# Optimization experiments

Measured on AMD Instinct MI355X. Metric: run time of the kernel, lower is better.

## Reference

```python
import jax, jax.numpy as jnp
import numpy as np

DIM = 1024
EXPERT_DIM = 2048
N_EXPERTS = 2
B, T = 4, 2048


def setup_inputs() -> dict:
    key = jax.random.key(0)
    ks = jax.random.split(key, 10)
    s = 0.02
    return {
        "x": jax.random.normal(ks[0], (B, T, DIM), dtype=jnp.float32),
        "W_router": jax.random.normal(ks[1], (DIM, N_EXPERTS), dtype=jnp.float32) * s,
        "router_bias": jnp.zeros((N_EXPERTS,), dtype=jnp.float32),
        "Wg": jax.random.normal(ks[2], (N_EXPERTS, DIM, EXPERT_DIM), dtype=jnp.float32) * s,
        "Wu": jax.random.normal(ks[3], (N_EXPERTS, DIM, EXPERT_DIM), dtype=jnp.float32) * s,
        "Wd": jax.random.normal(ks[4], (N_EXPERTS, EXPERT_DIM, DIM), dtype=jnp.float32) * s,
        "Sg": jax.random.normal(ks[5], (DIM, EXPERT_DIM), dtype=jnp.float32) * s,
        "Su": jax.random.normal(ks[6], (DIM, EXPERT_DIM), dtype=jnp.float32) * s,
        "Sd": jax.random.normal(ks[7], (EXPERT_DIM, DIM), dtype=jnp.float32) * s,
    }


def reference(x, W_router, router_bias, Wg, Wu, Wd, Sg, Su, Sd):
    Bc, Tc, D = x.shape
    flat = x.reshape(Bc * Tc, D)                               # [N, D]
    logits = flat @ W_router                                   # [N, E]
    scores = jax.nn.softmax(logits, axis=-1)
    hard = jax.nn.one_hot(jnp.argmax(logits + router_bias, axis=-1),
                          W_router.shape[1], dtype=flat.dtype)  # [N, E]
    # straight-through weights: forward value == hard, grad flows via scores
    ste = hard + scores - jax.lax.stop_gradient(scores)
    w = jnp.where(hard > 0.5, ste, jnp.zeros_like(ste))         # mask w > 0.5 (== argmax expert)
    # routed SwiGLU experts (top-1 hard routing; unselected rows weighted 0)
    g = jax.nn.silu(jnp.einsum('nd,edf->enf', flat, Wg))        # [E, N, F]
    u = jnp.einsum('nd,edf->enf', flat, Wu)
    y = jnp.einsum('enf,efd->end', g * u, Wd)                   # [E, N, D]
    routed = jnp.einsum('ne,end->nd', w, y)                     # [N, D]
    # always-active shared SwiGLU expert
    shared = (jax.nn.silu(flat @ Sg) * (flat @ Su)) @ Sd        # [N, D]
    return (routed + shared).reshape(Bc, Tc, D)
```

## Files before the change

### kernel.cpp

```cpp
#include <hip/hip_runtime.h>
#include <stdint.h>

#define NTOK 8192
#define DIM 1024
#define EDIM 2048

typedef __attribute__((ext_vector_type(8))) short bf16x8;
typedef __attribute__((ext_vector_type(4))) float f32x4;

__device__ __forceinline__ unsigned short f2bf(float f) {
  union { float f; unsigned u; } v; v.f = f;
  unsigned r = (v.u + 0x7FFF + ((v.u >> 16) & 1)) >> 16;
  return (unsigned short)r;
}

__device__ __forceinline__ void gload16(const void* g, void* l) {
  __builtin_amdgcn_global_load_lds(
      (const __attribute__((address_space(1))) unsigned int*)g,
      (__attribute__((address_space(3))) unsigned int*)l, 16, 0, 0);
}

__global__ void cvtrouter_k(const float* __restrict__ x, const float* __restrict__ Wr,
                            const float* __restrict__ bias,
                            unsigned short* __restrict__ xb, int* __restrict__ choice) {
  const int wid = threadIdx.x >> 6, lane = threadIdx.x & 63;
  const float b0 = bias[0], b1 = bias[1];
  const float2* wr = (const float2*)Wr;
  #pragma unroll
  for (int r = 0; r < 2; ++r) {
    const int n = blockIdx.x * 8 + wid * 2 + r;
    const float4* xr = (const float4*)(x + (size_t)n * DIM);
    uint2* xo = (uint2*)(xb + (size_t)n * DIM);
    float s0 = 0.f, s1 = 0.f;
    #pragma unroll
    for (int i = 0; i < 4; ++i) {
      const int idx = i * 64 + lane;
      float4 v = xr[idx];
      float2 wa = wr[idx * 4], wb = wr[idx * 4 + 1], wc = wr[idx * 4 + 2], wd = wr[idx * 4 + 3];
      s0 += v.x * wa.x + v.y * wb.x + v.z * wc.x + v.w * wd.x;
      s1 += v.x * wa.y + v.y * wb.y + v.z * wc.y + v.w * wd.y;
      union { unsigned short s[4]; uint2 u; } o;
      o.s[0] = f2bf(v.x); o.s[1] = f2bf(v.y); o.s[2] = f2bf(v.z); o.s[3] = f2bf(v.w);
      xo[idx] = o.u;
    }
    #pragma unroll
    for (int off = 32; off; off >>= 1) {
      s0 += __shfl_xor(s0, off);
      s1 += __shfl_xor(s1, off);
    }
    if (lane == 0) choice[n] = (s1 + b1 > s0 + b0) ? 1 : 0;
  }
}

__global__ void scan_k(const int* __restrict__ choice, int* __restrict__ counts,
                       int* __restrict__ rowlist) {
  const int t = threadIdx.x;
  const int base = t * 8;
  int c[8]; int ones = 0;
  #pragma unroll
  for (int j = 0; j < 8; ++j) { c[j] = choice[base + j]; ones += c[j]; }
  const int lane = t & 63, wid = t >> 6;
  int v = ones;
  #pragma unroll
  for (int off = 1; off < 64; off <<= 1) {
    int o = __shfl_up(v, off);
    if (lane >= off) v += o;
  }
  __shared__ int wsum[16];
  if (lane == 63) wsum[wid] = v;
  __syncthreads();
  int pre = 0, tot = 0;
  #pragma unroll
  for (int w = 0; w < 16; ++w) {
    int s = wsum[w];
    if (w < wid) pre += s;
    tot += s;
  }
  const int excl = pre + v - ones;
  int p0 = base - excl;
  int p1 = excl;
  #pragma unroll
  for (int j = 0; j < 8; ++j) {
    if (c[j]) rowlist[NTOK + p1++] = base + j;
    else rowlist[p0++] = base + j;
  }
  if (t == 0) { counts[0] = NTOK - tot; counts[1] = tot; }
}

__global__ void trans_k(const float* __restrict__ Sg, const float* __restrict__ Su,
                        const float* __restrict__ Sd, const float* __restrict__ Wg,
                        const float* __restrict__ Wu, const float* __restrict__ Wd,
                        unsigned short* __restrict__ wt) {
  const int id = blockIdx.y;
  const size_t MSZ = (size_t)DIM * EDIM;
  const float* src; int R, C;
  switch (id) {
    case 0: src = Sg;       R = DIM;  C = EDIM; break;
    case 1: src = Su;       R = DIM;  C = EDIM; break;
    case 2: src = Sd;       R = EDIM; C = DIM;  break;
    case 3: src = Wg;       R = DIM;  C = EDIM; break;
    case 4: src = Wg + MSZ; R = DIM;  C = EDIM; break;
    case 5: src = Wu;       R = DIM;  C = EDIM; break;
    case 6: src = Wu + MSZ; R = DIM;  C = EDIM; break;
    case 7: src = Wd;       R = EDIM; C = DIM;  break;
    default: src = Wd + MSZ; R = EDIM; C = DIM;  break;
  }
  unsigned short* dst = wt + (size_t)id * MSZ;
  __shared__ float tile[32][33];
  int tC = C >> 5;
  int tr = blockIdx.x / tC, tc = blockIdx.x % tC;
  int xt = threadIdx.x, yt = threadIdx.y;
  #pragma unroll
  for (int j = 0; j < 4; ++j)
    tile[yt + j * 8][xt] = src[(size_t)(tr * 32 + yt + j * 8) * C + tc * 32 + xt];
  __syncthreads();
  #pragma unroll
  for (int j = 0; j < 4; ++j)
    dst[(size_t)(tc * 32 + yt + j * 8) * R + tr * 32 + xt] = f2bf(tile[xt][yt + j * 8]);
}

template<bool GATHER>
__global__ __launch_bounds__(256, 2)
void up_k(const unsigned short* __restrict__ xb, const unsigned short* __restrict__ Bg0,
          const unsigned short* __restrict__ Bu0, const int* __restrict__ counts,
          const int* __restrict__ rowlist, unsigned short* __restrict__ h) {
  int mt, cnt;
  const int* rl = nullptr;
  const unsigned short* Bg = Bg0;
  const unsigned short* Bu = Bu0;
  if (GATHER) {
    int e = blockIdx.x >> 6;
    mt = blockIdx.x & 63;
    cnt = counts[e];
    if (mt * 128 >= cnt) return;
    rl = rowlist + e * NTOK;
    size_t off = (size_t)e * ((size_t)DIM * EDIM);
    Bg = Bg0 + off; Bu = Bu0 + off;
  } else { mt = blockIdx.x; cnt = NTOK; }

  const int t = threadIdx.x;
  const int lane = t & 63;
  const int wm = t >> 7, wn = (t >> 6) & 1;
  const int m0 = mt * 128, n0 = blockIdx.y * 128;

  __shared__ __align__(16) unsigned char lA[16384];
  __shared__ __align__(16) unsigned char lBg[16384];
  __shared__ __align__(16) unsigned char lBu[16384];

  size_t aoff[4], boff[4];
  int dsto[4];
  #pragma unroll
  for (int i = 0; i < 4; ++i) {
    int flat = i * 4096 + t * 16;
    int row = flat >> 7;
    int kb = (flat & 127) ^ ((row & 7) << 4);
    int ar = m0 + row;
    if (GATHER) ar = rl[ar < cnt ? ar : cnt - 1];
    aoff[i] = (size_t)ar * (DIM * 2) + kb;
    boff[i] = (size_t)(n0 + row) * (DIM * 2) + kb;
    dsto[i] = flat;
  }

  f32x4 accg[4][4], accu[4][4];
  #pragma unroll
  for (int i = 0; i < 4; ++i)
    #pragma unroll
    for (int j = 0; j < 4; ++j) {
      accg[i][j] = f32x4{0.f, 0.f, 0.f, 0.f};
      accu[i][j] = f32x4{0.f, 0.f, 0.f, 0.f};
    }

  const char* xc = (const char*)xb;
  const char* gc = (const char*)Bg;
  const char* uc = (const char*)Bu;

  for (int kt = 0; kt < DIM / 64; ++kt) {
    __syncthreads();
    size_t ko = (size_t)kt * 128;
    #pragma unroll
    for (int i = 0; i < 4; ++i) {
      gload16(xc + aoff[i] + ko, lA + dsto[i]);
      gload16(gc + boff[i] + ko, lBg + dsto[i]);
      gload16(uc + boff[i] + ko, lBu + dsto[i]);
    }
    __syncthreads();
    #pragma unroll
    for (int ks = 0; ks < 2; ++ks) {
      bf16x8 af[4], bgf[4], buf_[4];
      int kb = ks * 64 + ((lane >> 4) << 4);
      #pragma unroll
      for (int mi = 0; mi < 4; ++mi) {
        int row = wm * 64 + mi * 16 + (lane & 15);
        af[mi] = *(const bf16x8*)(lA + row * 128 + (kb ^ ((row & 7) << 4)));
      }
      #pragma unroll
      for (int ni = 0; ni < 4; ++ni) {
        int col = wn * 64 + ni * 16 + (lane & 15);
        int o = col * 128 + (kb ^ ((col & 7) << 4));
        bgf[ni] = *(const bf16x8*)(lBg + o);
        buf_[ni] = *(const bf16x8*)(lBu + o);
      }
      #pragma unroll
      for (int mi = 0; mi < 4; ++mi)
        #pragma unroll
        for (int ni = 0; ni < 4; ++ni) {
          accg[mi][ni] = __builtin_amdgcn_mfma_f32_16x16x32_bf16(af[mi], bgf[ni], accg[mi][ni], 0, 0, 0);
          accu[mi][ni] = __builtin_amdgcn_mfma_f32_16x16x32_bf16(af[mi], buf_[ni], accu[mi][ni], 0, 0, 0);
        }
    }
  }

  #pragma unroll
  for (int mi = 0; mi < 4; ++mi) {
    #pragma unroll
    for (int r = 0; r < 4; ++r) {
      int pr = m0 + wm * 64 + mi * 16 + ((lane >> 4) << 2) + r;
      if (GATHER && pr >= cnt) continue;
      int tok = GATHER ? rl[pr] : pr;
      unsigned short* hrow = h + (size_t)tok * EDIM;
      #pragma unroll
      for (int ni = 0; ni < 4; ++ni) {
        int col = n0 + wn * 64 + ni * 16 + (lane & 15);
        float g = accg[mi][ni][r], u = accu[mi][ni][r];
        float s = g / (1.f + __expf(-g));
        hrow[col] = f2bf(s * u);
      }
    }
  }
}

template<bool GATHER>
__global__ __launch_bounds__(256, 2)
void down_k(const unsigned short* __restrict__ hb, const unsigned short* __restrict__ Bd0,
            const int* __restrict__ counts, const int* __restrict__ rowlist,
            float* __restrict__ out) {
  int mt, cnt;
  const int* rl = nullptr;
  const unsigned short* Bd = Bd0;
  if (GATHER) {
    int e = blockIdx.x >> 6;
    mt = blockIdx.x & 63;
    cnt = counts[e];
    if (mt * 128 >= cnt) return;
    rl = rowlist + e * NTOK;
    Bd = Bd0 + (size_t)e * ((size_t)DIM * EDIM);
  } else { mt = blockIdx.x; cnt = NTOK; }

  const int t = threadIdx.x;
  const int lane = t & 63;
  const int wm = t >> 7, wn = (t >> 6) & 1;
  const int m0 = mt * 128, n0 = blockIdx.y * 128;

  __shared__ __align__(16) unsigned char lA[16384];
  __shared__ __align__(16) unsigned char lB[16384];

  size_t aoff[4], boff[4];
  int dsto[4];
  #pragma unroll
  for (int i = 0; i < 4; ++i) {
    int flat = i * 4096 + t * 16;
    int row = flat >> 7;
    int kb = (flat & 127) ^ ((row & 7) << 4);
    int ar = m0 + row;
    if (GATHER) ar = rl[ar < cnt ? ar : cnt - 1];
    aoff[i] = (size_t)ar * (EDIM * 2) + kb;
    boff[i] = (size_t)(n0 + row) * (EDIM * 2) + kb;
    dsto[i] = flat;
  }

  f32x4 acc[4][4];
  #pragma unroll
  for (int i = 0; i < 4; ++i)
    #pragma unroll
    for (int j = 0; j < 4; ++j) acc[i][j] = f32x4{0.f, 0.f, 0.f, 0.f};

  const char* ac = (const char*)hb;
  const char* bc = (const char*)Bd;

  for (int kt = 0; kt < EDIM / 64; ++kt) {
    __syncthreads();
    size_t ko = (size_t)kt * 128;
    #pragma unroll
    for (int i = 0; i < 4; ++i) {
      gload16(ac + aoff[i] + ko, lA + dsto[i]);
      gload16(bc + boff[i] + ko, lB + dsto[i]);
    }
    __syncthreads();
    #pragma unroll
    for (int ks = 0; ks < 2; ++ks) {
      bf16x8 af[4], bf[4];
      int kb = ks * 64 + ((lane >> 4) << 4);
      #pragma unroll
      for (int mi = 0; mi < 4; ++mi) {
        int row = wm * 64 + mi * 16 + (lane & 15);
        af[mi] = *(const bf16x8*)(lA + row * 128 + (kb ^ ((row & 7) << 4)));
      }
      #pragma unroll
      for (int ni = 0; ni < 4; ++ni) {
        int col = wn * 64 + ni * 16 + (lane & 15);
        bf[ni] = *(const bf16x8*)(lB + col * 128 + (kb ^ ((col & 7) << 4)));
      }
      #pragma unroll
      for (int mi = 0; mi < 4; ++mi)
        #pragma unroll
        for (int ni = 0; ni < 4; ++ni)
          acc[mi][ni] = __builtin_amdgcn_mfma_f32_16x16x32_bf16(af[mi], bf[ni], acc[mi][ni], 0, 0, 0);
    }
  }

  #pragma unroll
  for (int mi = 0; mi < 4; ++mi) {
    #pragma unroll
    for (int r = 0; r < 4; ++r) {
      int pr = m0 + wm * 64 + mi * 16 + ((lane >> 4) << 2) + r;
      if (GATHER && pr >= cnt) continue;
      int tok = GATHER ? rl[pr] : pr;
      float* orow = out + (size_t)tok * DIM;
      #pragma unroll
      for (int ni = 0; ni < 4; ++ni) {
        int col = n0 + wn * 64 + ni * 16 + (lane & 15);
        float v = acc[mi][ni][r];
        if (GATHER) orow[col] += v; else orow[col] = v;
      }
    }
  }
}

extern "C" void kernel_launch(void* const* d_in, const int* in_sizes, int n_in,
                              void* d_out, int out_size, void* d_ws, size_t ws_size,
                              hipStream_t stream) {
  const float* x  = (const float*)d_in[0];
  const float* Wr = (const float*)d_in[1];
  const float* rb = (const float*)d_in[2];
  const float* Wg = (const float*)d_in[3];
  const float* Wu = (const float*)d_in[4];
  const float* Wd = (const float*)d_in[5];
  const float* Sg = (const float*)d_in[6];
  const float* Su = (const float*)d_in[7];
  const float* Sd = (const float*)d_in[8];
  float* out = (float*)d_out;

  const size_t MSZ = (size_t)DIM * EDIM;
  char* ws = (char*)d_ws;
  int* counts  = (int*)ws;
  int* choice  = (int*)(ws + 256);
  int* rowlist = (int*)(ws + 256 + 32768);
  unsigned short* xb = (unsigned short*)(ws + 256 + 32768 + 65536);
  unsigned short* wt = xb + (size_t)NTOK * DIM;
  unsigned short* h  = wt + 9 * MSZ;

  const unsigned short* Sgt = wt + 0 * MSZ;
  const unsigned short* Sut = wt + 1 * MSZ;
  const unsigned short* Sdt = wt + 2 * MSZ;
  const unsigned short* Wgt = wt + 3 * MSZ;
  const unsigned short* Wut = wt + 5 * MSZ;
  const unsigned short* Wdt = wt + 7 * MSZ;

  cvtrouter_k<<<1024, 256, 0, stream>>>(x, Wr, rb, xb, choice);
  scan_k<<<1, 1024, 0, stream>>>(choice, counts, rowlist);
  trans_k<<<dim3(2048, 9), dim3(32, 8), 0, stream>>>(Sg, Su, Sd, Wg, Wu, Wd, wt);

  up_k<false><<<dim3(64, 16), 256, 0, stream>>>(xb, Sgt, Sut, nullptr, nullptr, h);
  down_k<false><<<dim3(64, 8), 256, 0, stream>>>(h, Sdt, nullptr, nullptr, out);
  up_k<true><<<dim3(128, 16), 256, 0, stream>>>(xb, Wgt, Wut, counts, rowlist, h);
  down_k<true><<<dim3(128, 8), 256, 0, stream>>>(h, Wdt, counts, rowlist, out);
}
```

Measured before the change: 284.3 us.

## Replace GEMM kernels with double-buffered 256-row tiled kernel and interleaved gate/up weights

```diff
diff --git a/kernel.cpp b/kernel.cpp
--- a/kernel.cpp
+++ b/kernel.cpp
@@ -19,6 +19,9 @@
       (const __attribute__((address_space(1))) unsigned int*)g,
       (__attribute__((address_space(3))) unsigned int*)l, 16, 0, 0);
 }
+
+#define BARRIER() do { __builtin_amdgcn_s_barrier(); asm volatile("" ::: "memory"); } while (0)
+#define VMW(n) asm volatile("s_waitcnt vmcnt(" #n ")" ::: "memory")
 
 __global__ void cvtrouter_k(const float* __restrict__ x, const float* __restrict__ Wr,
                             const float* __restrict__ bias,
@@ -93,19 +96,19 @@
                         unsigned short* __restrict__ wt) {
   const int id = blockIdx.y;
   const size_t MSZ = (size_t)DIM * EDIM;
-  const float* src; int R, C;
+  const float* src; int R, C, type; size_t dof;
   switch (id) {
-    case 0: src = Sg;       R = DIM;  C = EDIM; break;
-    case 1: src = Su;       R = DIM;  C = EDIM; break;
-    case 2: src = Sd;       R = EDIM; C = DIM;  break;
-    case 3: src = Wg;       R = DIM;  C = EDIM; break;
-    case 4: src = Wg + MSZ; R = DIM;  C = EDIM; break;
-    case 5: src = Wu;       R = DIM;  C = EDIM; break;
-    case 6: src = Wu + MSZ; R = DIM;  C = EDIM; break;
-    case 7: src = Wd;       R = EDIM; C = DIM;  break;
-    default: src = Wd + MSZ; R = EDIM; C = DIM;  break;
-  }
-  unsigned short* dst = wt + (size_t)id * MSZ;
+    case 0: src = Sg;       R = DIM;  C = EDIM; type = 0; dof = 0;        break;
+    case 1: src = Su;       R = DIM;  C = EDIM; type = 1; dof = 0;        break;
+    case 2: src = Wg;       R = DIM;  C = EDIM; type = 0; dof = 2 * MSZ;  break;
+    case 3: src = Wu;       R = DIM;  C = EDIM; type = 1; dof = 2 * MSZ;  break;
+    case 4: src = Wg + MSZ; R = DIM;  C = EDIM; type = 0; dof = 4 * MSZ;  break;
+    case 5: src = Wu + MSZ; R = DIM;  C = EDIM; type = 1; dof = 4 * MSZ;  break;
+    case 6: src = Sd;       R = EDIM; C = DIM;  type = 2; dof = 6 * MSZ;  break;
+    case 7: src = Wd;       R = EDIM; C = DIM;  type = 2; dof = 7 * MSZ;  break;
+    default: src = Wd + MSZ; R = EDIM; C = DIM; type = 2; dof = 8 * MSZ;  break;
+  }
+  unsigned short* dst = wt + dof;
   __shared__ float tile[32][33];
   int tC = C >> 5;
   int tr = blockIdx.x / tC, tc = blockIdx.x % tC;
@@ -115,212 +118,207 @@
     tile[yt + j * 8][xt] = src[(size_t)(tr * 32 + yt + j * 8) * C + tc * 32 + xt];
   __syncthreads();
   #pragma unroll
-  for (int j = 0; j < 4; ++j)
-    dst[(size_t)(tc * 32 + yt + j * 8) * R + tr * 32 + xt] = f2bf(tile[xt][yt + j * 8]);
-}
-
-template<bool GATHER>
-__global__ __launch_bounds__(256, 2)
-void up_k(const unsigned short* __restrict__ xb, const unsigned short* __restrict__ Bg0,
-          const unsigned short* __restrict__ Bu0, const int* __restrict__ counts,
-          const int* __restrict__ rowlist, unsigned short* __restrict__ h) {
-  int mt, cnt;
+  for (int j = 0; j < 4; ++j) {
+    int f = tc * 32 + yt + j * 8;
+    int row = (type == 2) ? f : (((f >> 4) << 5) + (f & 15) + (type ? 16 : 0));
+    dst[(size_t)row * R + tr * 32 + xt] = f2bf(tile[xt][yt + j * 8]);
+  }
+}
+
+template<int BN, int KDIM, bool GATHER, int EPI>
+__global__ __launch_bounds__(512, 2)
+void gemm_k(const unsigned short* __restrict__ A, const unsigned short* __restrict__ B0,
+            const int* __restrict__ counts, const int* __restrict__ rowlist,
+            unsigned short* __restrict__ hout, float* __restrict__ out) {
+  constexpr int NT = KDIM / 64;
+  constexpr int MROWS = (BN == 256) ? 128 : 64;
+  constexpr int MF = MROWS / 32;
+  constexpr int LB = BN / 128;
+  constexpr int BSUB = BN * 64;
+  constexpr int ROWB = KDIM * 2;
+
+  int m0, cnt = NTOK, mstart = 0;
   const int* rl = nullptr;
-  const unsigned short* Bg = Bg0;
-  const unsigned short* Bu = Bu0;
-  if (GATHER) {
-    int e = blockIdx.x >> 6;
-    mt = blockIdx.x & 63;
+  const unsigned short* B = B0;
+  if (EPI == 0 && GATHER) {
+    int e = blockIdx.x >> 5, mt = blockIdx.x & 31;
     cnt = counts[e];
-    if (mt * 128 >= cnt) return;
+    if (mt * 256 >= cnt) return;
     rl = rowlist + e * NTOK;
-    size_t off = (size_t)e * ((size_t)DIM * EDIM);
-    Bg = Bg0 + off; Bu = Bu0 + off;
-  } else { mt = blockIdx.x; cnt = NTOK; }
-
-  const int t = threadIdx.x;
-  const int lane = t & 63;
-  const int wm = t >> 7, wn = (t >> 6) & 1;
-  const int m0 = mt * 128, n0 = blockIdx.y * 128;
-
-  __shared__ __align__(16) unsigned char lA[16384];
-  __shared__ __align__(16) unsigned char lBg[16384];
-  __shared__ __align__(16) unsigned char lBu[16384];
-
-  size_t aoff[4], boff[4];
-  int dsto[4];
-  #pragma unroll
-  for (int i = 0; i < 4; ++i) {
-    int flat = i * 4096 + t * 16;
-    int row = flat >> 7;
-    int kb = (flat & 127) ^ ((row & 7) << 4);
-    int ar = m0 + row;
-    if (GATHER) ar = rl[ar < cnt ? ar : cnt - 1];
-    aoff[i] = (size_t)ar * (DIM * 2) + kb;
-    boff[i] = (size_t)(n0 + row) * (DIM * 2) + kb;
-    dsto[i] = flat;
-  }
-
-  f32x4 accg[4][4], accu[4][4];
-  #pragma unroll
-  for (int i = 0; i < 4; ++i)
-    #pragma unroll
-    for (int j = 0; j < 4; ++j) {
-      accg[i][j] = f32x4{0.f, 0.f, 0.f, 0.f};
-      accu[i][j] = f32x4{0.f, 0.f, 0.f, 0.f};
-    }
-
-  const char* xc = (const char*)xb;
-  const char* gc = (const char*)Bg;
-  const char* uc = (const char*)Bu;
-
-  for (int kt = 0; kt < DIM / 64; ++kt) {
-    __syncthreads();
-    size_t ko = (size_t)kt * 128;
-    #pragma unroll
-    for (int i = 0; i < 4; ++i) {
-      gload16(xc + aoff[i] + ko, lA + dsto[i]);
-      gload16(gc + boff[i] + ko, lBg + dsto[i]);
-      gload16(uc + boff[i] + ko, lBu + dsto[i]);
-    }
-    __syncthreads();
-    #pragma unroll
-    for (int ks = 0; ks < 2; ++ks) {
-      bf16x8 af[4], bgf[4], buf_[4];
-      int kb = ks * 64 + ((lane >> 4) << 4);
-      #pragma unroll
-      for (int mi = 0; mi < 4; ++mi) {
-        int row = wm * 64 + mi * 16 + (lane & 15);
-        af[mi] = *(const bf16x8*)(lA + row * 128 + (kb ^ ((row & 7) << 4)));
-      }
-      #pragma unroll
-      for (int ni = 0; ni < 4; ++ni) {
-        int col = wn * 64 + ni * 16 + (lane & 15);
-        int o = col * 128 + (kb ^ ((col & 7) << 4));
-        bgf[ni] = *(const bf16x8*)(lBg + o);
-        buf_[ni] = *(const bf16x8*)(lBu + o);
-      }
-      #pragma unroll
-      for (int mi = 0; mi < 4; ++mi)
-        #pragma unroll
-        for (int ni = 0; ni < 4; ++ni) {
-          accg[mi][ni] = __builtin_amdgcn_mfma_f32_16x16x32_bf16(af[mi], bgf[ni], accg[mi][ni], 0, 0, 0);
-          accu[mi][ni] = __builtin_amdgcn_mfma_f32_16x16x32_bf16(af[mi], buf_[ni], accu[mi][ni], 0, 0, 0);
+    mstart = e ? counts[0] : 0;
+    m0 = mt * 256;
+    B = B0 + (size_t)e * (2u * (size_t)DIM * EDIM);
+  } else if (EPI == 2) {
+    int e = blockIdx.x >> 5, mt = blockIdx.x & 31;
+    cnt = counts[e];
+    if (mt * 256 >= cnt) return;
+    rl = rowlist + e * NTOK;
+    mstart = e ? counts[0] : 0;
+    m0 = mstart + mt * 256;
+    B = B0 + (size_t)e * ((size_t)DIM * EDIM);
+  } else {
+    m0 = blockIdx.x * 256;
+  }
+  const int n0 = blockIdx.y * BN;
+
+  __shared__ __align__(16) unsigned char ldsA[65536];
+  __shared__ __align__(16) unsigned char ldsB[4 * BSUB];
+
+  const int t_ = threadIdx.x;
+  const int lane = t_ & 63;
+  const int wid = t_ >> 6;
+  const int wm = (BN == 256) ? (wid >> 2) : (wid >> 1);
+  const int wn = (BN == 256) ? (wid & 3) : (wid & 1);
+  const int l15 = lane & 15, l4 = lane >> 4;
+
+  uint32_t srcA[2]; int dstA[2];
+  #pragma unroll
+  for (int i = 0; i < 2; ++i) {
+    int line = i * 64 + (t_ >> 3);
+    int sl = (t_ & 7) ^ (line & 7);
+    int ra = 2 * line + (sl >> 2), kc = sl & 3;
+    int grow;
+    if (EPI == 0 && GATHER) {
+      int idx = m0 + ra; if (idx >= cnt) idx = cnt - 1;
+      grow = rl[idx];
+    } else {
+      grow = m0 + ra; if (grow > NTOK - 1) grow = NTOK - 1;
+    }
+    srcA[i] = (uint32_t)grow * ROWB + kc * 16;
+    dstA[i] = i * 8192 + t_ * 16;
+  }
+  uint32_t srcB[LB]; int dstB[LB];
+  #pragma unroll
+  for (int i = 0; i < LB; ++i) {
+    int line = i * 64 + (t_ >> 3);
+    int sl = (t_ & 7) ^ (line & 7);
+    int rb = 2 * line + (sl >> 2), kc = sl & 3;
+    srcB[i] = (uint32_t)(n0 + rb) * ROWB + kc * 16;
+    dstB[i] = i * 8192 + t_ * 16;
+  }
+
+  const char* Ab = (const char*)A;
+  const char* Bb = (const char*)B;
+  auto issueA = [&](int kt, int kh) {
+    if (kt >= NT) return;
+    char* dst = (char*)ldsA + ((kt & 1) * 2 + kh) * 16384;
+    #pragma unroll
+    for (int i = 0; i < 2; ++i)
+      gload16(Ab + srcA[i] + kt * 128 + kh * 64, dst + dstA[i]);
+  };
+  auto issueB = [&](int kt, int kh) {
+    if (kt >= NT) return;
+    char* dst = (char*)ldsB + ((kt & 1) * 2 + kh) * BSUB;
+    #pragma unroll
+    for (int i = 0; i < LB; ++i)
+      gload16(Bb + srcB[i] + kt * 128 + kh * 64, dst + dstB[i]);
+  };
+  auto ldfrag = [&](const unsigned char* sub, int row) -> bf16x8 {
+    int line = row >> 1;
+    int s = (((row & 1) << 2) | l4) ^ (line & 7);
+    return *(const bf16x8*)(sub + line * 128 + s * 16);
+  };
+
+  f32x4 acc[2 * MF][4];
+  #pragma unroll
+  for (int i = 0; i < 2 * MF; ++i)
+    #pragma unroll
+    for (int j = 0; j < 4; ++j) acc[i][j] = f32x4{0.f, 0.f, 0.f, 0.f};
+
+  issueA(0, 0); issueB(0, 0); issueA(0, 1); issueB(0, 1);
+  if (BN == 256) { VMW(4); } else { VMW(3); }
+  BARRIER();
+
+  for (int kt = 0; kt < NT; ++kt) {
+    const unsigned char* As0 = ldsA + ((kt & 1) * 2 + 0) * 16384;
+    const unsigned char* As1 = ldsA + ((kt & 1) * 2 + 1) * 16384;
+    const unsigned char* Bs0 = ldsB + ((kt & 1) * 2 + 0) * BSUB;
+    const unsigned char* Bs1 = ldsB + ((kt & 1) * 2 + 1) * BSUB;
+    bf16x8 aR[MF], bR[4];
+    #pragma unroll
+    for (int m = 0; m < MF; ++m) aR[m] = ldfrag(As0, wm * MROWS + m * 16 + l15);
+    #pragma unroll
+    for (int n = 0; n < 4; ++n) bR[n] = ldfrag(Bs0, wn * 64 + n * 16 + l15);
+    issueA(kt + 1, 0);
+    __builtin_amdgcn_s_setprio(1);
+    #pragma unroll
+    for (int m = 0; m < MF; ++m)
+      #pragma unroll
+      for (int n = 0; n < 4; ++n)
+        acc[m][n] = __builtin_amdgcn_mfma_f32_16x16x32_bf16(aR[m], bR[n], acc[m][n], 0, 0, 0);
+    __builtin_amdgcn_s_setprio(0);
+    BARRIER();
+    #pragma unroll
+    for (int m = 0; m < MF; ++m) aR[m] = ldfrag(As0, wm * MROWS + MROWS / 2 + m * 16 + l15);
+    issueB(kt + 1, 0);
+    __builtin_amdgcn_s_setprio(1);
+    #pragma unroll
+    for (int m = 0; m < MF; ++m)
+      #pragma unroll
+      for (int n = 0; n < 4; ++n)
+        acc[MF + m][n] = __builtin_amdgcn_mfma_f32_16x16x32_bf16(aR[m], bR[n], acc[MF + m][n], 0, 0, 0);
+    __builtin_amdgcn_s_setprio(0);
+    if (kt + 1 < NT) { if (BN == 256) { VMW(4); } else { VMW(3); } } else { VMW(0); }
+    BARRIER();
+    #pragma unroll
+    for (int m = 0; m < MF; ++m) aR[m] = ldfrag(As1, wm * MROWS + m * 16 + l15);
+    #pragma unroll
+    for (int n = 0; n < 4; ++n) bR[n] = ldfrag(Bs1, wn * 64 + n * 16 + l15);
+    issueA(kt + 1, 1);
+    __builtin_amdgcn_s_setprio(1);
+    #pragma unroll
+    for (int m = 0; m < MF; ++m)
+      #pragma unroll
+      for (int n = 0; n < 4; ++n)
+        acc[m][n] = __builtin_amdgcn_mfma_f32_16x16x32_bf16(aR[m], bR[n], acc[m][n], 0, 0, 0);
+    __builtin_amdgcn_s_setprio(0);
+    BARRIER();
+    #pragma unroll
+    for (int m = 0; m < MF; ++m) aR[m] = ldfrag(As1, wm * MROWS + MROWS / 2 + m * 16 + l15);
+    issueB(kt + 1, 1);
+    __builtin_amdgcn_s_setprio(1);
+    #pragma unroll
+    for (int m = 0; m < MF; ++m)
+      #pragma unroll
+      for (int n = 0; n < 4; ++n)
+        acc[MF + m][n] = __builtin_amdgcn_mfma_f32_16x16x32_bf16(aR[m], bR[n], acc[MF + m][n], 0, 0, 0);
+    __builtin_amdgcn_s_setprio(0);
+    if (kt + 1 < NT) {
+      if (BN == 256) { VMW(4); } else { VMW(3); }
+      BARRIER();
+    }
+  }
+
+  #pragma unroll
+  for (int ch = 0; ch < 2; ++ch) {
+    #pragma unroll
+    for (int m = 0; m < MF; ++m) {
+      #pragma unroll
+      for (int r = 0; r < 4; ++r) {
+        const int rit = wm * MROWS + ch * (MROWS / 2) + m * 16 + l4 * 4 + r;
+        if (EPI == 0) {
+          const int pos = m0 + rit;
+          if (GATHER && pos >= cnt) continue;
+          unsigned short* hr = hout + (size_t)(mstart + pos) * EDIM;
+          const int f0 = (n0 >> 1) + wn * 32;
+          float g = acc[ch * MF + m][0][r], u = acc[ch * MF + m][1][r];
+          hr[f0 + l15] = f2bf(g / (1.f + __expf(-g)) * u);
+          g = acc[ch * MF + m][2][r]; u = acc[ch * MF + m][3][r];
+          hr[f0 + 16 + l15] = f2bf(g / (1.f + __expf(-g)) * u);
+        } else if (EPI == 1) {
+          float* orow = out + (size_t)(m0 + rit) * DIM;
+          #pragma unroll
+          for (int n = 0; n < 4; ++n)
+            orow[n0 + wn * 64 + n * 16 + l15] = acc[ch * MF + m][n][r];
+        } else {
+          const int idxe = (m0 - mstart) + rit;
+          if (idxe >= cnt) continue;
+          const int tok = rl[idxe];
+          float* orow = out + (size_t)tok * DIM;
+          #pragma unroll
+          for (int n = 0; n < 4; ++n)
+            orow[n0 + wn * 64 + n * 16 + l15] += acc[ch * MF + m][n][r];
         }
-    }
-  }
-
-  #pragma unroll
-  for (int mi = 0; mi < 4; ++mi) {
-    #pragma unroll
-    for (int r = 0; r < 4; ++r) {
-      int pr = m0 + wm * 64 + mi * 16 + ((lane >> 4) << 2) + r;
-      if (GATHER && pr >= cnt) continue;
-      int tok = GATHER ? rl[pr] : pr;
-      unsigned short* hrow = h + (size_t)tok * EDIM;
-      #pragma unroll
-      for (int ni = 0; ni < 4; ++ni) {
-        int col = n0 + wn * 64 + ni * 16 + (lane & 15);
-        float g = accg[mi][ni][r], u = accu[mi][ni][r];
-        float s = g / (1.f + __expf(-g));
-        hrow[col] = f2bf(s * u);
-      }
-    }
-  }
-}
-
-template<bool GATHER>
-__global__ __launch_bounds__(256, 2)
-void down_k(const unsigned short* __restrict__ hb, const unsigned short* __restrict__ Bd0,
-            const int* __restrict__ counts, const int* __restrict__ rowlist,
-            float* __restrict__ out) {
-  int mt, cnt;
-  const int* rl = nullptr;
-  const unsigned short* Bd = Bd0;
-  if (GATHER) {
-    int e = blockIdx.x >> 6;
-    mt = blockIdx.x & 63;
-    cnt = counts[e];
-    if (mt * 128 >= cnt) return;
-    rl = rowlist + e * NTOK;
-    Bd = Bd0 + (size_t)e * ((size_t)DIM * EDIM);
-  } else { mt = blockIdx.x; cnt = NTOK; }
-
-  const int t = threadIdx.x;
-  const int lane = t & 63;
-  const int wm = t >> 7, wn = (t >> 6) & 1;
-  const int m0 = mt * 128, n0 = blockIdx.y * 128;
-
-  __shared__ __align__(16) unsigned char lA[16384];
-  __shared__ __align__(16) unsigned char lB[16384];
-
-  size_t aoff[4], boff[4];
-  int dsto[4];
-  #pragma unroll
-  for (int i = 0; i < 4; ++i) {
-    int flat = i * 4096 + t * 16;
-    int row = flat >> 7;
-    int kb = (flat & 127) ^ ((row & 7) << 4);
-    int ar = m0 + row;
-    if (GATHER) ar = rl[ar < cnt ? ar : cnt - 1];
-    aoff[i] = (size_t)ar * (EDIM * 2) + kb;
-    boff[i] = (size_t)(n0 + row) * (EDIM * 2) + kb;
-    dsto[i] = flat;
-  }
-
-  f32x4 acc[4][4];
-  #pragma unroll
-  for (int i = 0; i < 4; ++i)
-    #pragma unroll
-    for (int j = 0; j < 4; ++j) acc[i][j] = f32x4{0.f, 0.f, 0.f, 0.f};
-
-  const char* ac = (const char*)hb;
-  const char* bc = (const char*)Bd;
-
-  for (int kt = 0; kt < EDIM / 64; ++kt) {
-    __syncthreads();
-    size_t ko = (size_t)kt * 128;
-    #pragma unroll
-    for (int i = 0; i < 4; ++i) {
-      gload16(ac + aoff[i] + ko, lA + dsto[i]);
-      gload16(bc + boff[i] + ko, lB + dsto[i]);
-    }
-    __syncthreads();
-    #pragma unroll
-    for (int ks = 0; ks < 2; ++ks) {
-      bf16x8 af[4], bf[4];
-      int kb = ks * 64 + ((lane >> 4) << 4);
-      #pragma unroll
-      for (int mi = 0; mi < 4; ++mi) {
-        int row = wm * 64 + mi * 16 + (lane & 15);
-        af[mi] = *(const bf16x8*)(lA + row * 128 + (kb ^ ((row & 7) << 4)));
-      }
-      #pragma unroll
-      for (int ni = 0; ni < 4; ++ni) {
-        int col = wn * 64 + ni * 16 + (lane & 15);
-        bf[ni] = *(const bf16x8*)(lB + col * 128 + (kb ^ ((col & 7) << 4)));
-      }
-      #pragma unroll
-      for (int mi = 0; mi < 4; ++mi)
-        #pragma unroll
-        for (int ni = 0; ni < 4; ++ni)
-          acc[mi][ni] = __builtin_amdgcn_mfma_f32_16x16x32_bf16(af[mi], bf[ni], acc[mi][ni], 0, 0, 0);
-    }
-  }
-
-  #pragma unroll
-  for (int mi = 0; mi < 4; ++mi) {
-    #pragma unroll
-    for (int r = 0; r < 4; ++r) {
-      int pr = m0 + wm * 64 + mi * 16 + ((lane >> 4) << 2) + r;
-      if (GATHER && pr >= cnt) continue;
-      int tok = GATHER ? rl[pr] : pr;
-      float* orow = out + (size_t)tok * DIM;
-      #pragma unroll
-      for (int ni = 0; ni < 4; ++ni) {
-        int col = n0 + wn * 64 + ni * 16 + (lane & 15);
-        float v = acc[mi][ni][r];
-        if (GATHER) orow[col] += v; else orow[col] = v;
       }
     }
   }
@@ -349,19 +347,17 @@
   unsigned short* wt = xb + (size_t)NTOK * DIM;
   unsigned short* h  = wt + 9 * MSZ;
 
-  const unsigned short* Sgt = wt + 0 * MSZ;
-  const unsigned short* Sut = wt + 1 * MSZ;
-  const unsigned short* Sdt = wt + 2 * MSZ;
-  const unsigned short* Wgt = wt + 3 * MSZ;
-  const unsigned short* Wut = wt + 5 * MSZ;
+  const unsigned short* Sgu = wt;
+  const unsigned short* Wgu = wt + 2 * MSZ;
+  const unsigned short* Sdt = wt + 6 * MSZ;
   const unsigned short* Wdt = wt + 7 * MSZ;
 
   cvtrouter_k<<<1024, 256, 0, stream>>>(x, Wr, rb, xb, choice);
   scan_k<<<1, 1024, 0, stream>>>(choice, counts, rowlist);
   trans_k<<<dim3(2048, 9), dim3(32, 8), 0, stream>>>(Sg, Su, Sd, Wg, Wu, Wd, wt);
 
-  up_k<false><<<dim3(64, 16), 256, 0, stream>>>(xb, Sgt, Sut, nullptr, nullptr, h);
-  down_k<false><<<dim3(64, 8), 256, 0, stream>>>(h, Sdt, nullptr, nullptr, out);
-  up_k<true><<<dim3(128, 16), 256, 0, stream>>>(xb, Wgt, Wut, counts, rowlist, h);
-  down_k<true><<<dim3(128, 8), 256, 0, stream>>>(h, Wdt, counts, rowlist, out);
-}
+  gemm_k<256, DIM, false, 0><<<dim3(32, 16), 512, 0, stream>>>(xb, Sgu, counts, rowlist, h, nullptr);
+  gemm_k<128, EDIM, false, 1><<<dim3(32, 8), 512, 0, stream>>>(h, Sdt, counts, rowlist, nullptr, out);
+  gemm_k<256, DIM, true, 0><<<dim3(64, 16), 512, 0, stream>>>(xb, Wgu, counts, rowlist, h, nullptr);
+  gemm_k<128, EDIM, false, 2><<<dim3(64, 8), 512, 0, stream>>>(h, Wdt, counts, rowlist, nullptr, out);
+}
```

After: 385.2 us. 35.5% more time.

## Interleave gate/up weights into one GEMM, fuse prep kernels, compact expert rows

Applied to the files above, without the earlier changes.

```diff
diff --git a/kernel.cpp b/kernel.cpp
--- a/kernel.cpp
+++ b/kernel.cpp
@@ -20,35 +20,81 @@
       (__attribute__((address_space(3))) unsigned int*)l, 16, 0, 0);
 }
 
-__global__ void cvtrouter_k(const float* __restrict__ x, const float* __restrict__ Wr,
-                            const float* __restrict__ bias,
-                            unsigned short* __restrict__ xb, int* __restrict__ choice) {
-  const int wid = threadIdx.x >> 6, lane = threadIdx.x & 63;
-  const float b0 = bias[0], b1 = bias[1];
-  const float2* wr = (const float2*)Wr;
-  #pragma unroll
-  for (int r = 0; r < 2; ++r) {
-    const int n = blockIdx.x * 8 + wid * 2 + r;
-    const float4* xr = (const float4*)(x + (size_t)n * DIM);
-    uint2* xo = (uint2*)(xb + (size_t)n * DIM);
-    float s0 = 0.f, s1 = 0.f;
-    #pragma unroll
-    for (int i = 0; i < 4; ++i) {
-      const int idx = i * 64 + lane;
-      float4 v = xr[idx];
-      float2 wa = wr[idx * 4], wb = wr[idx * 4 + 1], wc = wr[idx * 4 + 2], wd = wr[idx * 4 + 3];
-      s0 += v.x * wa.x + v.y * wb.x + v.z * wc.x + v.w * wd.x;
-      s1 += v.x * wa.y + v.y * wb.y + v.z * wc.y + v.w * wd.y;
-      union { unsigned short s[4]; uint2 u; } o;
-      o.s[0] = f2bf(v.x); o.s[1] = f2bf(v.y); o.s[2] = f2bf(v.z); o.s[3] = f2bf(v.w);
-      xo[idx] = o.u;
-    }
-    #pragma unroll
-    for (int off = 32; off; off >>= 1) {
-      s0 += __shfl_xor(s0, off);
-      s1 += __shfl_xor(s1, off);
-    }
-    if (lane == 0) choice[n] = (s1 + b1 > s0 + b0) ? 1 : 0;
+__global__ void pre_k(const float* __restrict__ x, const float* __restrict__ Wr,
+                      const float* __restrict__ bias,
+                      const float* __restrict__ Sg, const float* __restrict__ Su,
+                      const float* __restrict__ Sd, const float* __restrict__ Wg,
+                      const float* __restrict__ Wu, const float* __restrict__ Wd,
+                      unsigned short* __restrict__ xb, int* __restrict__ choice,
+                      unsigned short* __restrict__ wt) {
+  const int bx = blockIdx.x;
+  const int t = threadIdx.x;
+  const size_t MSZ = (size_t)DIM * EDIM;
+  if (bx < 1024) {
+    const int wid = t >> 6, lane = t & 63;
+    const float b0 = bias[0], b1 = bias[1];
+    const float2* wr = (const float2*)Wr;
+    #pragma unroll
+    for (int r = 0; r < 2; ++r) {
+      const int n = bx * 8 + wid * 2 + r;
+      const float4* xr = (const float4*)(x + (size_t)n * DIM);
+      uint2* xo = (uint2*)(xb + (size_t)n * DIM);
+      float s0 = 0.f, s1 = 0.f;
+      #pragma unroll
+      for (int i = 0; i < 4; ++i) {
+        const int idx = i * 64 + lane;
+        float4 v = xr[idx];
+        float2 wa = wr[idx * 4], wb = wr[idx * 4 + 1], wc = wr[idx * 4 + 2], wd = wr[idx * 4 + 3];
+        s0 += v.x * wa.x + v.y * wb.x + v.z * wc.x + v.w * wd.x;
+        s1 += v.x * wa.y + v.y * wb.y + v.z * wc.y + v.w * wd.y;
+        union { unsigned short s[4]; uint2 u; } o;
+        o.s[0] = f2bf(v.x); o.s[1] = f2bf(v.y); o.s[2] = f2bf(v.z); o.s[3] = f2bf(v.w);
+        xo[idx] = o.u;
+      }
+      #pragma unroll
+      for (int off = 32; off; off >>= 1) {
+        s0 += __shfl_xor(s0, off);
+        s1 += __shfl_xor(s1, off);
+      }
+      if (lane == 0) choice[n] = (s1 + b1 > s0 + b0) ? 1 : 0;
+    }
+    return;
+  }
+  const int id = bx - 1024;
+  const int mat = id >> 11;
+  const int tile = id & 2047;
+  const float* src; unsigned short* dst; int type;
+  switch (mat) {
+    case 0: src = Sg;       dst = wt;            type = 0; break;
+    case 1: src = Su;       dst = wt;            type = 1; break;
+    case 2: src = Wg;       dst = wt + 4194304;  type = 0; break;
+    case 3: src = Wu;       dst = wt + 4194304;  type = 1; break;
+    case 4: src = Wg + MSZ; dst = wt + 8388608;  type = 0; break;
+    case 5: src = Wu + MSZ; dst = wt + 8388608;  type = 1; break;
+    case 6: src = Sd;       dst = wt + 12582912; type = 2; break;
+    case 7: src = Wd;       dst = wt + 14680064; type = 2; break;
+    default: src = Wd + MSZ; dst = wt + 16777216; type = 2; break;
+  }
+  const int R = (type == 2) ? EDIM : DIM;
+  const int C = (type == 2) ? DIM : EDIM;
+  __shared__ float ts[32][33];
+  const int tC = C >> 5;
+  const int tr = tile / tC, tc = tile % tC;
+  const int xt = t & 31, yt = t >> 5;
+  #pragma unroll
+  for (int j = 0; j < 4; ++j)
+    ts[yt + j * 8][xt] = src[(size_t)(tr * 32 + yt + j * 8) * C + tc * 32 + xt];
+  __syncthreads();
+  #pragma unroll
+  for (int j = 0; j < 4; ++j) {
+    const int cc = tc * 32 + yt + j * 8;
+    const int rr = tr * 32 + xt;
+    const float v = ts[xt][yt + j * 8];
+    if (type == 2) dst[(size_t)cc * EDIM + rr] = f2bf(v);
+    else {
+      const int row = ((cc >> 4) << 5) + (cc & 15) + (type << 4);
+      dst[(size_t)row * DIM + rr] = f2bf(v);
+    }
   }
 }
 
@@ -77,227 +123,101 @@
     tot += s;
   }
   const int excl = pre + v - ones;
+  const int cnt0 = NTOK - tot;
   int p0 = base - excl;
-  int p1 = excl;
+  int p1 = cnt0 + excl;
   #pragma unroll
   for (int j = 0; j < 8; ++j) {
-    if (c[j]) rowlist[NTOK + p1++] = base + j;
+    if (c[j]) rowlist[p1++] = base + j;
     else rowlist[p0++] = base + j;
   }
-  if (t == 0) { counts[0] = NTOK - tot; counts[1] = tot; }
-}
-
-__global__ void trans_k(const float* __restrict__ Sg, const float* __restrict__ Su,
-                        const float* __restrict__ Sd, const float* __restrict__ Wg,
-                        const float* __restrict__ Wu, const float* __restrict__ Wd,
-                        unsigned short* __restrict__ wt) {
-  const int id = blockIdx.y;
-  const size_t MSZ = (size_t)DIM * EDIM;
-  const float* src; int R, C;
-  switch (id) {
-    case 0: src = Sg;       R = DIM;  C = EDIM; break;
-    case 1: src = Su;       R = DIM;  C = EDIM; break;
-    case 2: src = Sd;       R = EDIM; C = DIM;  break;
-    case 3: src = Wg;       R = DIM;  C = EDIM; break;
-    case 4: src = Wg + MSZ; R = DIM;  C = EDIM; break;
-    case 5: src = Wu;       R = DIM;  C = EDIM; break;
-    case 6: src = Wu + MSZ; R = DIM;  C = EDIM; break;
-    case 7: src = Wd;       R = EDIM; C = DIM;  break;
-    default: src = Wd + MSZ; R = EDIM; C = DIM;  break;
-  }
-  unsigned short* dst = wt + (size_t)id * MSZ;
-  __shared__ float tile[32][33];
-  int tC = C >> 5;
-  int tr = blockIdx.x / tC, tc = blockIdx.x % tC;
-  int xt = threadIdx.x, yt = threadIdx.y;
-  #pragma unroll
-  for (int j = 0; j < 4; ++j)
-    tile[yt + j * 8][xt] = src[(size_t)(tr * 32 + yt + j * 8) * C + tc * 32 + xt];
-  __syncthreads();
-  #pragma unroll
-  for (int j = 0; j < 4; ++j)
-    dst[(size_t)(tc * 32 + yt + j * 8) * R + tr * 32 + xt] = f2bf(tile[xt][yt + j * 8]);
-}
-
-template<bool GATHER>
-__global__ __launch_bounds__(256, 2)
-void up_k(const unsigned short* __restrict__ xb, const unsigned short* __restrict__ Bg0,
-          const unsigned short* __restrict__ Bu0, const int* __restrict__ counts,
-          const int* __restrict__ rowlist, unsigned short* __restrict__ h) {
-  int mt, cnt;
-  const int* rl = nullptr;
-  const unsigned short* Bg = Bg0;
-  const unsigned short* Bu = Bu0;
-  if (GATHER) {
-    int e = blockIdx.x >> 6;
-    mt = blockIdx.x & 63;
-    cnt = counts[e];
-    if (mt * 128 >= cnt) return;
-    rl = rowlist + e * NTOK;
-    size_t off = (size_t)e * ((size_t)DIM * EDIM);
-    Bg = Bg0 + off; Bu = Bu0 + off;
-  } else { mt = blockIdx.x; cnt = NTOK; }
+  if (t == 0) { counts[0] = cnt0; counts[1] = tot; }
+}
+
+template<int KDIM, int MODE>
+__global__ __launch_bounds__(256, 4)
+void gemm2_k(const unsigned short* __restrict__ A, const unsigned short* __restrict__ B0,
+             const int* __restrict__ counts, const int* __restrict__ rl,
+             unsigned short* __restrict__ h, float* __restrict__ out) {
+  constexpr int NT = KDIM / 64;
+  constexpr int ROWB = KDIM * 2;
+
+  int e = 0, mstart = 0, cntE = NTOK, r0;
+  if (MODE == 1 || MODE == 3) {
+    e = blockIdx.x >> 6;
+    const int mt = blockIdx.x & 63;
+    const int c0 = counts[0];
+    cntE = e ? (NTOK - c0) : c0;
+    mstart = e ? c0 : 0;
+    r0 = mt * 128;
+    if (r0 >= cntE) return;
+  } else {
+    r0 = blockIdx.x * 128;
+  }
+  const int n0 = blockIdx.y * 128;
+  const unsigned short* B = B0;
+  if (MODE == 1) B += (size_t)e * 4194304u;
+  if (MODE == 3) B += (size_t)e * 2097152u;
+
+  __shared__ __align__(16) unsigned char lA[16384];
+  __shared__ __align__(16) unsigned char lB[16384];
 
   const int t = threadIdx.x;
   const int lane = t & 63;
   const int wm = t >> 7, wn = (t >> 6) & 1;
-  const int m0 = mt * 128, n0 = blockIdx.y * 128;
-
-  __shared__ __align__(16) unsigned char lA[16384];
-  __shared__ __align__(16) unsigned char lBg[16384];
-  __shared__ __align__(16) unsigned char lBu[16384];
-
-  size_t aoff[4], boff[4];
-  int dsto[4];
+  const int l15 = lane & 15, l4 = lane >> 4;
+
+  size_t aoff[4]; uint32_t boff[4]; int dsto[4];
   #pragma unroll
   for (int i = 0; i < 4; ++i) {
-    int flat = i * 4096 + t * 16;
-    int row = flat >> 7;
-    int kb = (flat & 127) ^ ((row & 7) << 4);
-    int ar = m0 + row;
-    if (GATHER) ar = rl[ar < cnt ? ar : cnt - 1];
-    aoff[i] = (size_t)ar * (DIM * 2) + kb;
-    boff[i] = (size_t)(n0 + row) * (DIM * 2) + kb;
+    const int flat = i * 4096 + t * 16;
+    const int row = flat >> 7;
+    const int kb = (flat & 127) ^ ((row & 7) << 4);
+    int ar;
+    if (MODE == 1) {
+      int idx = r0 + row; if (idx >= cntE) idx = cntE - 1;
+      ar = rl[mstart + idx];
+    } else if (MODE == 3) {
+      int idx = r0 + row; if (idx >= cntE) idx = cntE - 1;
+      ar = mstart + idx;
+    } else {
+      ar = r0 + row;
+    }
+    aoff[i] = (size_t)ar * ROWB + kb;
+    boff[i] = (uint32_t)(n0 + row) * ROWB + kb;
     dsto[i] = flat;
   }
 
-  f32x4 accg[4][4], accu[4][4];
+  f32x4 acc[4][4];
   #pragma unroll
   for (int i = 0; i < 4; ++i)
     #pragma unroll
-    for (int j = 0; j < 4; ++j) {
-      accg[i][j] = f32x4{0.f, 0.f, 0.f, 0.f};
-      accu[i][j] = f32x4{0.f, 0.f, 0.f, 0.f};
-    }
-
-  const char* xc = (const char*)xb;
-  const char* gc = (const char*)Bg;
-  const char* uc = (const char*)Bu;
-
-  for (int kt = 0; kt < DIM / 64; ++kt) {
+    for (int j = 0; j < 4; ++j) acc[i][j] = f32x4{0.f, 0.f, 0.f, 0.f};
+
+  const char* Ab = (const char*)A;
+  const char* Bb = (const char*)B;
+
+  for (int kt = 0; kt < NT; ++kt) {
     __syncthreads();
-    size_t ko = (size_t)kt * 128;
+    const size_t ko = (size_t)kt * 128;
     #pragma unroll
     for (int i = 0; i < 4; ++i) {
-      gload16(xc + aoff[i] + ko, lA + dsto[i]);
-      gload16(gc + boff[i] + ko, lBg + dsto[i]);
-      gload16(uc + boff[i] + ko, lBu + dsto[i]);
-    }
-    __syncthreads();
-    #pragma unroll
-    for (int ks = 0; ks < 2; ++ks) {
-      bf16x8 af[4], bgf[4], buf_[4];
-      int kb = ks * 64 + ((lane >> 4) << 4);
-      #pragma unroll
-      for (int mi = 0; mi < 4; ++mi) {
-        int row = wm * 64 + mi * 16 + (lane & 15);
-        af[mi] = *(const bf16x8*)(lA + row * 128 + (kb ^ ((row & 7) << 4)));
-      }
-      #pragma unroll
-      for (int ni = 0; ni < 4; ++ni) {
-        int col = wn * 64 + ni * 16 + (lane & 15);
-        int o = col * 128 + (kb ^ ((col & 7) << 4));
-        bgf[ni] = *(const bf16x8*)(lBg + o);
-        buf_[ni] = *(const bf16x8*)(lBu + o);
-      }
-      #pragma unroll
-      for (int mi = 0; mi < 4; ++mi)
-        #pragma unroll
-        for (int ni = 0; ni < 4; ++ni) {
-          accg[mi][ni] = __builtin_amdgcn_mfma_f32_16x16x32_bf16(af[mi], bgf[ni], accg[mi][ni], 0, 0, 0);
-          accu[mi][ni] = __builtin_amdgcn_mfma_f32_16x16x32_bf16(af[mi], buf_[ni], accu[mi][ni], 0, 0, 0);
-        }
-    }
-  }
-
-  #pragma unroll
-  for (int mi = 0; mi < 4; ++mi) {
-    #pragma unroll
-    for (int r = 0; r < 4; ++r) {
-      int pr = m0 + wm * 64 + mi * 16 + ((lane >> 4) << 2) + r;
-      if (GATHER && pr >= cnt) continue;
-      int tok = GATHER ? rl[pr] : pr;
-      unsigned short* hrow = h + (size_t)tok * EDIM;
-      #pragma unroll
-      for (int ni = 0; ni < 4; ++ni) {
-        int col = n0 + wn * 64 + ni * 16 + (lane & 15);
-        float g = accg[mi][ni][r], u = accu[mi][ni][r];
-        float s = g / (1.f + __expf(-g));
-        hrow[col] = f2bf(s * u);
-      }
-    }
-  }
-}
-
-template<bool GATHER>
-__global__ __launch_bounds__(256, 2)
-void down_k(const unsigned short* __restrict__ hb, const unsigned short* __restrict__ Bd0,
-            const int* __restrict__ counts, const int* __restrict__ rowlist,
-            float* __restrict__ out) {
-  int mt, cnt;
-  const int* rl = nullptr;
-  const unsigned short* Bd = Bd0;
-  if (GATHER) {
-    int e = blockIdx.x >> 6;
-    mt = blockIdx.x & 63;
-    cnt = counts[e];
-    if (mt * 128 >= cnt) return;
-    rl = rowlist + e * NTOK;
-    Bd = Bd0 + (size_t)e * ((size_t)DIM * EDIM);
-  } else { mt = blockIdx.x; cnt = NTOK; }
-
-  const int t = threadIdx.x;
-  const int lane = t & 63;
-  const int wm = t >> 7, wn = (t >> 6) & 1;
-  const int m0 = mt * 128, n0 = blockIdx.y * 128;
-
-  __shared__ __align__(16) unsigned char lA[16384];
-  __shared__ __align__(16) unsigned char lB[16384];
-
-  size_t aoff[4], boff[4];
-  int dsto[4];
-  #pragma unroll
-  for (int i = 0; i < 4; ++i) {
-    int flat = i * 4096 + t * 16;
-    int row = flat >> 7;
-    int kb = (flat & 127) ^ ((row & 7) << 4);
-    int ar = m0 + row;
-    if (GATHER) ar = rl[ar < cnt ? ar : cnt - 1];
-    aoff[i] = (size_t)ar * (EDIM * 2) + kb;
-    boff[i] = (size_t)(n0 + row) * (EDIM * 2) + kb;
-    dsto[i] = flat;
-  }
-
-  f32x4 acc[4][4];
-  #pragma unroll
-  for (int i = 0; i < 4; ++i)
-    #pragma unroll
-    for (int j = 0; j < 4; ++j) acc[i][j] = f32x4{0.f, 0.f, 0.f, 0.f};
-
-  const char* ac = (const char*)hb;
-  const char* bc = (const char*)Bd;
-
-  for (int kt = 0; kt < EDIM / 64; ++kt) {
-    __syncthreads();
-    size_t ko = (size_t)kt * 128;
-    #pragma unroll
-    for (int i = 0; i < 4; ++i) {
-      gload16(ac + aoff[i] + ko, lA + dsto[i]);
-      gload16(bc + boff[i] + ko, lB + dsto[i]);
+      gload16(Ab + aoff[i] + ko, lA + dsto[i]);
+      gload16(Bb + boff[i] + ko, lB + dsto[i]);
     }
     __syncthreads();
     #pragma unroll
     for (int ks = 0; ks < 2; ++ks) {
       bf16x8 af[4], bf[4];
-      int kb = ks * 64 + ((lane >> 4) << 4);
+      const int kb = ks * 64 + (l4 << 4);
       #pragma unroll
       for (int mi = 0; mi < 4; ++mi) {
-        int row = wm * 64 + mi * 16 + (lane & 15);
+        const int row = wm * 64 + mi * 16 + l15;
         af[mi] = *(const bf16x8*)(lA + row * 128 + (kb ^ ((row & 7) << 4)));
       }
       #pragma unroll
       for (int ni = 0; ni < 4; ++ni) {
-        int col = wn * 64 + ni * 16 + (lane & 15);
+        const int col = wn * 64 + ni * 16 + l15;
         bf[ni] = *(const bf16x8*)(lB + col * 128 + (kb ^ ((col & 7) << 4)));
       }
       #pragma unroll
@@ -312,15 +232,30 @@
   for (int mi = 0; mi < 4; ++mi) {
     #pragma unroll
     for (int r = 0; r < 4; ++r) {
-      int pr = m0 + wm * 64 + mi * 16 + ((lane >> 4) << 2) + r;
-      if (GATHER && pr >= cnt) continue;
-      int tok = GATHER ? rl[pr] : pr;
-      float* orow = out + (size_t)tok * DIM;
-      #pragma unroll
-      for (int ni = 0; ni < 4; ++ni) {
-        int col = n0 + wn * 64 + ni * 16 + (lane & 15);
-        float v = acc[mi][ni][r];
-        if (GATHER) orow[col] += v; else orow[col] = v;
+      const int rit = wm * 64 + mi * 16 + l4 * 4 + r;
+      if (MODE == 0 || MODE == 1) {
+        const int pos = r0 + rit;
+        if (MODE == 1 && pos >= cntE) continue;
+        unsigned short* hr = h + (size_t)(mstart + pos) * EDIM;
+        const int f0 = (n0 >> 1) + wn * 32;
+        #pragma unroll
+        for (int j = 0; j < 2; ++j) {
+          const float g = acc[mi][2 * j][r], u = acc[mi][2 * j + 1][r];
+          hr[f0 + j * 16 + l15] = f2bf(g / (1.f + __expf(-g)) * u);
+        }
+      } else if (MODE == 2) {
+        float* orow = out + (size_t)(r0 + rit) * DIM;
+        #pragma unroll
+        for (int n = 0; n < 4; ++n)
+          orow[n0 + wn * 64 + n * 16 + l15] = acc[mi][n][r];
+      } else {
+        const int pos = r0 + rit;
+        if (pos >= cntE) continue;
+        const int tok = rl[mstart + pos];
+        float* orow = out + (size_t)tok * DIM;
+        #pragma unroll
+        for (int n = 0; n < 4; ++n)
+          orow[n0 + wn * 64 + n * 16 + l15] += acc[mi][n][r];
       }
     }
   }
@@ -340,28 +275,25 @@
   const float* Sd = (const float*)d_in[8];
   float* out = (float*)d_out;
 
-  const size_t MSZ = (size_t)DIM * EDIM;
   char* ws = (char*)d_ws;
   int* counts  = (int*)ws;
   int* choice  = (int*)(ws + 256);
   int* rowlist = (int*)(ws + 256 + 32768);
-  unsigned short* xb = (unsigned short*)(ws + 256 + 32768 + 65536);
+  unsigned short* xb = (unsigned short*)(ws + 256 + 65536);
   unsigned short* wt = xb + (size_t)NTOK * DIM;
-  unsigned short* h  = wt + 9 * MSZ;
-
-  const unsigned short* Sgt = wt + 0 * MSZ;
-  const unsigned short* Sut = wt + 1 * MSZ;
-  const unsigned short* Sdt = wt + 2 * MSZ;
-  const unsigned short* Wgt = wt + 3 * MSZ;
-  const unsigned short* Wut = wt + 5 * MSZ;
-  const unsigned short* Wdt = wt + 7 * MSZ;
-
-  cvtrouter_k<<<1024, 256, 0, stream>>>(x, Wr, rb, xb, choice);
+  unsigned short* h  = wt + 18874368;
+
+  const unsigned short* Sgu  = wt;
+  const unsigned short* Wgu0 = wt + 4194304;
+  const unsigned short* Sdt  = wt + 12582912;
+  const unsigned short* Wdt0 = wt + 14680064;
+
+  pre_k<<<1024 + 9 * 2048, 256, 0, stream>>>(x, Wr, rb, Sg, Su, Sd, Wg, Wu, Wd,
+                                             xb, choice, wt);
   scan_k<<<1, 1024, 0, stream>>>(choice, counts, rowlist);
-  trans_k<<<dim3(2048, 9), dim3(32, 8), 0, stream>>>(Sg, Su, Sd, Wg, Wu, Wd, wt);
-
-  up_k<false><<<dim3(64, 16), 256, 0, stream>>>(xb, Sgt, Sut, nullptr, nullptr, h);
-  down_k<false><<<dim3(64, 8), 256, 0, stream>>>(h, Sdt, nullptr, nullptr, out);
-  up_k<true><<<dim3(128, 16), 256, 0, stream>>>(xb, Wgt, Wut, counts, rowlist, h);
-  down_k<true><<<dim3(128, 8), 256, 0, stream>>>(h, Wdt, counts, rowlist, out);
-}
+
+  gemm2_k<DIM, 0><<<dim3(64, 32), 256, 0, stream>>>(xb, Sgu, counts, rowlist, h, nullptr);
+  gemm2_k<EDIM, 2><<<dim3(64, 8), 256, 0, stream>>>(h, Sdt, counts, rowlist, nullptr, out);
+  gemm2_k<DIM, 1><<<dim3(128, 32), 256, 0, stream>>>(xb, Wgu0, counts, rowlist, h, nullptr);
+  gemm2_k<EDIM, 3><<<dim3(128, 8), 256, 0, stream>>>(h, Wdt0, counts, rowlist, nullptr, out);
+}
```

Measured after the change: 280.3 us. About the same (-1.4%).
